# Kernel tuning notes

Measured on AMD Instinct MI355X. Metric: run time of the kernel, lower is better.

Reference implementation:

```python
import jax, jax.numpy as jnp
import numpy as np

N_NODES = 50000
N_EDGES = 800000
IN_FEATS = 128
NUM_HEADS = 4
OUT_FEATS = 16
NEG_SLOPE = 0.2


def setup_inputs() -> dict:
    key = jax.random.key(0)
    k_feat, k_src, k_dst, k_w, k_al, k_ar = jax.random.split(key, 6)
    feat = jax.random.normal(k_feat, (N_NODES, IN_FEATS), dtype=jnp.float32)
    src = jax.random.randint(k_src, (N_EDGES,), 0, N_NODES, dtype=jnp.int32)
    # guarantee every destination node has in-degree >= 1 (segment softmax well-defined)
    dst_rand = jax.random.randint(k_dst, (N_EDGES - N_NODES,), 0, N_NODES, dtype=jnp.int32)
    dst = jnp.concatenate([jnp.arange(N_NODES, dtype=jnp.int32), dst_rand])
    # xavier-normal-ish parameter scales
    W = jax.random.normal(k_w, (IN_FEATS, NUM_HEADS * OUT_FEATS), dtype=jnp.float32) * (
        1.414 * (2.0 / (IN_FEATS + NUM_HEADS * OUT_FEATS)) ** 0.5)
    attn_l = jax.random.normal(k_al, (NUM_HEADS, OUT_FEATS), dtype=jnp.float32) * 0.1
    attn_r = jax.random.normal(k_ar, (NUM_HEADS, OUT_FEATS), dtype=jnp.float32) * 0.1
    bias = jnp.zeros((NUM_HEADS * OUT_FEATS,), dtype=jnp.float32)
    return {"feat": feat, "src": src, "dst": dst, "W": W,
            "attn_l": attn_l, "attn_r": attn_r, "bias": bias}


def reference(feat, src, dst, W, attn_l, attn_r, bias):
    N = feat.shape[0]
    H, D = attn_l.shape
    # shared projection (homogeneous-graph branch, eval mode: dropout = identity)
    ft = (feat @ W).reshape(N, H, D)                      # [N,H,D]
    el = jnp.einsum('nhd,hd->nh', ft, attn_l)             # [N,H]
    er = jnp.einsum('nhd,hd->nh', ft, attn_r)             # [N,H]
    # u_add_v + leaky_relu -> per-edge logits [E,H]
    e = jax.nn.leaky_relu(el[src] + er[dst], negative_slope=NEG_SLOPE)
    # edge_softmax: stable segment softmax over destination neighborhoods
    m = jax.ops.segment_max(e, dst, num_segments=N)       # [N,H]
    ex = jnp.exp(e - m[dst])                              # [E,H]
    s = jax.ops.segment_sum(ex, dst, num_segments=N)      # [N,H]
    a = ex / s[dst]                                       # [E,H]
    # u_mul_e + sum: gather src features, weight, scatter-add to dst
    msg = ft[src] * a[:, :, None]                         # [E,H,D]
    rst = jax.ops.segment_sum(msg, dst, num_segments=N)   # [N,H,D]
    return rst + bias.reshape(1, H, D)
```

## Files before the change

kernel.cpp:

```cpp
#include <hip/hip_runtime.h>
#include <hip/hip_fp16.h>
#include <math.h>

#define IN_FEATS 128
#define HD 64
#define H 4
#define D 16
#define SLAB 64
#define NXCD 8
#define FILL_EPT 8
#define FILL_CHUNK (256 * FILL_EPT)

__global__ __launch_bounds__(256) void k_proj(
    const float* __restrict__ feat, const float* __restrict__ W,
    const float* __restrict__ attn_l, const float* __restrict__ attn_r,
    __half* __restrict__ ft16, float* __restrict__ el, float* __restrict__ er,
    int* __restrict__ cnt, int N)
{
    __shared__ float sW[IN_FEATS * HD];
    __shared__ float srow[16][IN_FEATS];

    const int tid = threadIdx.x;
    const int nbase = blockIdx.x * 16;

    if (tid < 16 && nbase + tid < N) cnt[nbase + tid] = 0;

    #pragma unroll
    for (int i = tid; i < IN_FEATS * HD / 4; i += 256)
        ((float4*)sW)[i] = ((const float4*)W)[i];

    #pragma unroll
    for (int i = tid; i < 16 * 32; i += 256) {
        int li   = i >> 5;
        int node = nbase + li;
        float4 v = (node < N) ? ((const float4*)feat)[(size_t)node * 32 + (i & 31)]
                              : make_float4(0.f, 0.f, 0.f, 0.f);
        ((float4*)&srow[li][0])[i & 31] = v;
    }
    __syncthreads();

    const int wid  = tid >> 6;
    const int lane = tid & 63;
    const int h    = lane >> 4;

    float acc[4] = {0.f, 0.f, 0.f, 0.f};
    #pragma unroll 8
    for (int k = 0; k < IN_FEATS; ++k) {
        float w = sW[k * HD + lane];
        #pragma unroll
        for (int q = 0; q < 4; ++q)
            acc[q] = fmaf(srow[wid * 4 + q][k], w, acc[q]);
    }

    const float wl = attn_l[lane];
    const float wr = attn_r[lane];
    #pragma unroll
    for (int q = 0; q < 4; ++q) {
        int node = nbase + wid * 4 + q;
        if (node >= N) break;
        float a = acc[q];
        ft16[(size_t)node * HD + lane] = __float2half(a);
        float l = a * wl, r = a * wr;
        #pragma unroll
        for (int off = 8; off >= 1; off >>= 1) {
            l += __shfl_xor(l, off, 16);
            r += __shfl_xor(r, off, 16);
        }
        if ((lane & 15) == 0) {
            el[node * H + h] = l;
            er[node * H + h] = r;
        }
    }
}

__global__ __launch_bounds__(256) void k_fill(
    const int* __restrict__ src, const int* __restrict__ dst,
    int* __restrict__ cnt, unsigned short* __restrict__ slab, int E, int R)
{
    const int xcd   = blockIdx.x & (NXCD - 1);
    const int chunk = blockIdx.x >> 3;
    const int dlo   = xcd * R;
    const int base  = chunk * FILL_CHUNK + threadIdx.x * FILL_EPT;

    if (base + FILL_EPT <= E) {
        int4 d0 = *(const int4*)(dst + base);
        int4 d1 = *(const int4*)(dst + base + 4);
        int4 s0 = *(const int4*)(src + base);
        int4 s1 = *(const int4*)(src + base + 4);
        int dd[FILL_EPT] = {d0.x, d0.y, d0.z, d0.w, d1.x, d1.y, d1.z, d1.w};
        int ss[FILL_EPT] = {s0.x, s0.y, s0.z, s0.w, s1.x, s1.y, s1.z, s1.w};
        #pragma unroll
        for (int i = 0; i < FILL_EPT; ++i) {
            int d = dd[i];
            if ((unsigned)(d - dlo) < (unsigned)R) {
                int p = atomicAdd(&cnt[d], 1);
                if (p < SLAB) slab[(size_t)d * SLAB + p] = (unsigned short)ss[i];
            }
        }
    } else {
        for (int e = base; e < E; ++e) {
            int d = dst[e];
            if ((unsigned)(d - dlo) < (unsigned)R) {
                int p = atomicAdd(&cnt[d], 1);
                if (p < SLAB) slab[(size_t)d * SLAB + p] = (unsigned short)src[e];
            }
        }
    }
}

__global__ __launch_bounds__(256) void k_aggregate(
    const __half* __restrict__ ft16, const float* __restrict__ el,
    const float* __restrict__ er, const int* __restrict__ cnt,
    const unsigned short* __restrict__ slab, const float* __restrict__ bias,
    float* __restrict__ out, int N, int R)
{
    const int tid = threadIdx.x;
    const int xcd = blockIdx.x & (NXCD - 1);
    const int loc = blockIdx.x >> 3;
    const int ln  = loc * 4 + (tid >> 6);
    if (ln >= R) return;
    const int n = xcd * R + ln;
    if (n >= N) return;

    const int lane = tid & 63;
    const int h    = lane >> 4;

    const float ern = er[n * H + h];
    const int deg = min(cnt[n], SLAB);
    const unsigned short* __restrict__ row = slab + (size_t)n * SLAB;

    float acc  = 0.f;
    float ssum = 0.f;

    for (int j = 0; j < deg; j += 8) {
        int4 a = *(const int4*)(row + j);

        int s0 = a.x & 0xFFFF;
        int s1 = (j + 1 < deg) ? ((a.x >> 16) & 0xFFFF) : s0;
        int s2 = (j + 2 < deg) ? (a.y & 0xFFFF)         : s0;
        int s3 = (j + 3 < deg) ? ((a.y >> 16) & 0xFFFF) : s0;
        int s4 = (j + 4 < deg) ? (a.z & 0xFFFF)         : s0;
        int s5 = (j + 5 < deg) ? ((a.z >> 16) & 0xFFFF) : s0;
        int s6 = (j + 6 < deg) ? (a.w & 0xFFFF)         : s0;
        int s7 = (j + 7 < deg) ? ((a.w >> 16) & 0xFFFF) : s0;

        float e0 = el[s0 * H + h];
        float e1 = el[s1 * H + h];
        float e2 = el[s2 * H + h];
        float e3 = el[s3 * H + h];
        float e4 = el[s4 * H + h];
        float e5 = el[s5 * H + h];
        float e6 = el[s6 * H + h];
        float e7 = el[s7 * H + h];

        float f0 = __half2float(ft16[(size_t)s0 * HD + lane]);
        float f1 = __half2float(ft16[(size_t)s1 * HD + lane]);
        float f2 = __half2float(ft16[(size_t)s2 * HD + lane]);
        float f3 = __half2float(ft16[(size_t)s3 * HD + lane]);
        float f4 = __half2float(ft16[(size_t)s4 * HD + lane]);
        float f5 = __half2float(ft16[(size_t)s5 * HD + lane]);
        float f6 = __half2float(ft16[(size_t)s6 * HD + lane]);
        float f7 = __half2float(ft16[(size_t)s7 * HD + lane]);

        e0 += ern; e0 = (e0 > 0.f) ? e0 : 0.2f * e0;
        e1 += ern; e1 = (e1 > 0.f) ? e1 : 0.2f * e1;
        e2 += ern; e2 = (e2 > 0.f) ? e2 : 0.2f * e2;
        e3 += ern; e3 = (e3 > 0.f) ? e3 : 0.2f * e3;
        e4 += ern; e4 = (e4 > 0.f) ? e4 : 0.2f * e4;
        e5 += ern; e5 = (e5 > 0.f) ? e5 : 0.2f * e5;
        e6 += ern; e6 = (e6 > 0.f) ? e6 : 0.2f * e6;
        e7 += ern; e7 = (e7 > 0.f) ? e7 : 0.2f * e7;

        float x0 = __expf(e0);
        float x1 = (j + 1 < deg) ? __expf(e1) : 0.f;
        float x2 = (j + 2 < deg) ? __expf(e2) : 0.f;
        float x3 = (j + 3 < deg) ? __expf(e3) : 0.f;
        float x4 = (j + 4 < deg) ? __expf(e4) : 0.f;
        float x5 = (j + 5 < deg) ? __expf(e5) : 0.f;
        float x6 = (j + 6 < deg) ? __expf(e6) : 0.f;
        float x7 = (j + 7 < deg) ? __expf(e7) : 0.f;

        ssum += ((x0 + x1) + (x2 + x3)) + ((x4 + x5) + (x6 + x7));
        acc = fmaf(x0, f0, acc);
        acc = fmaf(x1, f1, acc);
        acc = fmaf(x2, f2, acc);
        acc = fmaf(x3, f3, acc);
        acc = fmaf(x4, f4, acc);
        acc = fmaf(x5, f5, acc);
        acc = fmaf(x6, f6, acc);
        acc = fmaf(x7, f7, acc);
    }

    out[(size_t)n * HD + lane] = acc / ssum + bias[lane];
}

extern "C" void kernel_launch(void* const* d_in, const int* in_sizes, int n_in,
                              void* d_out, int out_size, void* d_ws, size_t ws_size,
                              hipStream_t stream)
{
    const float* feat   = (const float*)d_in[0];
    const int*   src    = (const int*)  d_in[1];
    const int*   dst    = (const int*)  d_in[2];
    const float* W      = (const float*)d_in[3];
    const float* attn_l = (const float*)d_in[4];
    const float* attn_r = (const float*)d_in[5];
    const float* bias   = (const float*)d_in[6];
    float*       out    = (float*)d_out;

    const int N = in_sizes[0] / IN_FEATS;
    const int E = in_sizes[1];
    const int R = (N + NXCD - 1) / NXCD;

    char* ws = (char*)d_ws;
    __half*         ft16 = (__half*)ws;         ws += (size_t)N * HD * sizeof(__half);
    float*          el   = (float*)ws;          ws += (size_t)N * H * sizeof(float);
    float*          er   = (float*)ws;          ws += (size_t)N * H * sizeof(float);
    int*            cnt  = (int*)ws;            ws += (size_t)N * sizeof(int);
    unsigned short* slab = (unsigned short*)ws;

    const int nchunks = (E + FILL_CHUNK - 1) / FILL_CHUNK;
    k_proj<<<(N + 15) / 16, 256, 0, stream>>>(feat, W, attn_l, attn_r,
                                              ft16, el, er, cnt, N);
    k_fill<<<nchunks * NXCD, 256, 0, stream>>>(src, dst, cnt, slab, E, R);
    k_aggregate<<<((R + 3) / 4) * NXCD, 256, 0, stream>>>(ft16, el, er, cnt,
                                                          slab, bias, out, N, R);
}
```

Before: 102.6 us.

## Compute node projection with bf16 MFMA instead of scalar LDS FMA loop

The projection kernel now gives each wavefront a 16-node tile and computes feat@W with 16x16x32 bf16 MFMA instructions. Feature rows and W columns are converted to bf16 in registers, which removes the shared-memory staging of W and the block-wide barrier. The attention dot products are then reduced from the MFMA output layout. This lowers precision of the projection to bf16 inputs, and each wave reloads W from global/L2 with strided scalar loads.

```diff
diff --git a/kernel.cpp b/kernel.cpp
--- a/kernel.cpp
+++ b/kernel.cpp
@@ -11,64 +11,81 @@
 #define FILL_EPT 8
 #define FILL_CHUNK (256 * FILL_EPT)
 
+typedef __attribute__((ext_vector_type(8))) short bf16x8;
+typedef __attribute__((ext_vector_type(4))) float f32x4;
+
+__device__ __forceinline__ short f2bf(float x) {
+    unsigned u = __float_as_uint(x);
+    u += 0x7FFFu + ((u >> 16) & 1u);
+    return (short)(u >> 16);
+}
+
 __global__ __launch_bounds__(256) void k_proj(
     const float* __restrict__ feat, const float* __restrict__ W,
     const float* __restrict__ attn_l, const float* __restrict__ attn_r,
     __half* __restrict__ ft16, float* __restrict__ el, float* __restrict__ er,
     int* __restrict__ cnt, int N)
 {
-    __shared__ float sW[IN_FEATS * HD];
-    __shared__ float srow[16][IN_FEATS];
-
-    const int tid = threadIdx.x;
-    const int nbase = blockIdx.x * 16;
-
-    if (tid < 16 && nbase + tid < N) cnt[nbase + tid] = 0;
-
+    const int tid   = threadIdx.x;
+    const int wid   = tid >> 6;
+    const int lane  = tid & 63;
+    const int nbase = (blockIdx.x * 4 + wid) * 16;
+    if (nbase >= N) return;
+
+    if (lane < 16 && nbase + lane < N) cnt[nbase + lane] = 0;
+
+    const int m = lane & 15;
+    const int g = lane >> 4;
+    const int arow = min(nbase + m, N - 1);
+
+    bf16x8 afrag[4];
+    const float* ap = feat + (size_t)arow * IN_FEATS + 8 * g;
     #pragma unroll
-    for (int i = tid; i < IN_FEATS * HD / 4; i += 256)
-        ((float4*)sW)[i] = ((const float4*)W)[i];
-
+    for (int s = 0; s < 4; ++s) {
+        float4 lo = *(const float4*)(ap + 32 * s);
+        float4 hi = *(const float4*)(ap + 32 * s + 4);
+        bf16x8 a;
+        a[0] = f2bf(lo.x); a[1] = f2bf(lo.y); a[2] = f2bf(lo.z); a[3] = f2bf(lo.w);
+        a[4] = f2bf(hi.x); a[5] = f2bf(hi.y); a[6] = f2bf(hi.z); a[7] = f2bf(hi.w);
+        afrag[s] = a;
+    }
+
+    f32x4 acc[4] = {{0.f,0.f,0.f,0.f}, {0.f,0.f,0.f,0.f},
+                    {0.f,0.f,0.f,0.f}, {0.f,0.f,0.f,0.f}};
     #pragma unroll
-    for (int i = tid; i < 16 * 32; i += 256) {
-        int li   = i >> 5;
-        int node = nbase + li;
-        float4 v = (node < N) ? ((const float4*)feat)[(size_t)node * 32 + (i & 31)]
-                              : make_float4(0.f, 0.f, 0.f, 0.f);
-        ((float4*)&srow[li][0])[i & 31] = v;
-    }
-    __syncthreads();
-
-    const int wid  = tid >> 6;
-    const int lane = tid & 63;
-    const int h    = lane >> 4;
-
-    float acc[4] = {0.f, 0.f, 0.f, 0.f};
-    #pragma unroll 8
-    for (int k = 0; k < IN_FEATS; ++k) {
-        float w = sW[k * HD + lane];
+    for (int s = 0; s < 4; ++s) {
+        const float* wp = W + (size_t)(32 * s + 8 * g) * HD + m;
         #pragma unroll
-        for (int q = 0; q < 4; ++q)
-            acc[q] = fmaf(srow[wid * 4 + q][k], w, acc[q]);
-    }
-
-    const float wl = attn_l[lane];
-    const float wr = attn_r[lane];
+        for (int c4 = 0; c4 < 4; ++c4) {
+            const float* bp = wp + 16 * c4;
+            bf16x8 b;
+            #pragma unroll
+            for (int j = 0; j < 8; ++j) b[j] = f2bf(bp[(size_t)j * HD]);
+            acc[c4] = __builtin_amdgcn_mfma_f32_16x16x32_bf16(
+                          afrag[s], b, acc[c4], 0, 0, 0);
+        }
+    }
+
     #pragma unroll
-    for (int q = 0; q < 4; ++q) {
-        int node = nbase + wid * 4 + q;
-        if (node >= N) break;
-        float a = acc[q];
-        ft16[(size_t)node * HD + lane] = __float2half(a);
-        float l = a * wl, r = a * wr;
+    for (int c4 = 0; c4 < 4; ++c4) {
+        const float al = attn_l[c4 * 16 + m];
+        const float ar = attn_r[c4 * 16 + m];
         #pragma unroll
-        for (int off = 8; off >= 1; off >>= 1) {
-            l += __shfl_xor(l, off, 16);
-            r += __shfl_xor(r, off, 16);
-        }
-        if ((lane & 15) == 0) {
-            el[node * H + h] = l;
-            er[node * H + h] = r;
+        for (int r = 0; r < 4; ++r) {
+            const int node = nbase + 4 * g + r;
+            float v = acc[c4][r];
+            if (node < N)
+                ft16[(size_t)node * HD + c4 * 16 + m] = __float2half(v);
+            float l = v * al, rr = v * ar;
+            #pragma unroll
+            for (int off = 8; off >= 1; off >>= 1) {
+                l  += __shfl_xor(l,  off, 16);
+                rr += __shfl_xor(rr, off, 16);
+            }
+            if (m == 0 && node < N) {
+                el[node * H + c4] = l;
+                er[node * H + c4] = rr;
+            }
         }
     }
 }
@@ -218,9 +235,10 @@
     int*            cnt  = (int*)ws;            ws += (size_t)N * sizeof(int);
     unsigned short* slab = (unsigned short*)ws;
 
+    const int ntiles  = (N + 15) / 16;
     const int nchunks = (E + FILL_CHUNK - 1) / FILL_CHUNK;
-    k_proj<<<(N + 15) / 16, 256, 0, stream>>>(feat, W, attn_l, attn_r,
-                                              ft16, el, er, cnt, N);
+    k_proj<<<(ntiles + 3) / 4, 256, 0, stream>>>(feat, W, attn_l, attn_r,
+                                                 ft16, el, er, cnt, N);
     k_fill<<<nchunks * NXCD, 256, 0, stream>>>(src, dst, cnt, slab, E, R);
     k_aggregate<<<((R + 3) / 4) * NXCD, 256, 0, stream>>>(ft16, el, er, cnt,
                                                           slab, bias, out, N, R);
```

After: 88.92 us. 13.3% less time.
